# Kernel optimization log

Measured on AMD Instinct MI355X. Metric: run time of the kernel, lower is better.

The kernel has to match this reference:

```python
import jax, jax.numpy as jnp
import numpy as np

HIDDEN = 1024
HEADS = 16
HEAD_DIM = HIDDEN // HEADS
B, S = 2, 1024


def setup_inputs() -> dict:
    key = jax.random.key(0)
    ks = jax.random.split(key, 14)
    sc = 1.0 / np.sqrt(HIDDEN)
    inp = {
        "q": jax.random.normal(ks[0], (B, S, HIDDEN), jnp.float32),
        "k": jax.random.normal(ks[1], (B, S, HIDDEN), jnp.float32),
        "v": jax.random.normal(ks[2], (B, S, HIDDEN), jnp.float32),
        "mask": jax.random.randint(ks[3], (B, S), 0, 2, jnp.int32),
        "shift": jax.random.normal(ks[4], (B * HEADS, S, S), jnp.float32) * 0.1,
        "wq": jax.random.normal(ks[5], (HIDDEN, HIDDEN), jnp.float32) * sc,
        "bq": jnp.zeros((HIDDEN,), jnp.float32),
        "wk": jax.random.normal(ks[6], (HIDDEN, HIDDEN), jnp.float32) * sc,
        "bk": jnp.zeros((HIDDEN,), jnp.float32),
        "wv": jax.random.normal(ks[7], (HIDDEN, HIDDEN), jnp.float32) * sc,
        "bv": jnp.zeros((HIDDEN,), jnp.float32),
        "wo": jax.random.normal(ks[8], (HIDDEN, HIDDEN), jnp.float32) * sc,
        "bo": jnp.zeros((HIDDEN,), jnp.float32),
    }
    return inp


def _to_heads(x):
    # (B,S,Dm) -> (B*H, S, Dh), batch-major over heads (b*H + h)
    b, s, _ = x.shape
    return x.reshape(b, s, HEADS, HEAD_DIM).transpose(0, 2, 1, 3).reshape(b * HEADS, s, HEAD_DIM)


def reference(q, k, v, mask, shift, wq, bq, wk, bk, wv, bv, wo, bo):
    b, s, dm = q.shape
    qh = _to_heads(q @ wq.T + bq)
    kh = _to_heads(k @ wk.T + bk)
    vh = _to_heads(v @ wv.T + bv)
    scores = jnp.einsum("bqd,bkd->bqk", qh, kh) / jnp.float32(np.sqrt(HEAD_DIM))
    scores = scores + shift
    # faithful to torch: mask tiled head-major (h*B + b) -> outer product m_i * m_j
    m = jnp.tile(mask, (HEADS, 1))  # (H*B, S)
    attn_mask = m[:, :, None] * m[:, None, :]  # (H*B, S, S)
    scores = jnp.where(attn_mask == 0, jnp.float32(-1e9), scores)
    p = jax.nn.softmax(scores, axis=-1)
    out = jnp.einsum("bqk,bkd->bqd", p, vh)
    out = out.reshape(b, HEADS, s, HEAD_DIM).transpose(0, 2, 1, 3).reshape(b, s, dm)
    return out @ wo.T + bo
```

## Files before the change

kernel.cpp:

```cpp
#include <hip/hip_runtime.h>
#include <hip/hip_bf16.h>

#define S_LEN 1024
#define DMODEL 1024
#define N_HEADS 16
#define D_HEAD 64
#define BATCH 2
#define N_BH 32

typedef __attribute__((ext_vector_type(8))) short short8;
typedef __attribute__((ext_vector_type(4))) float f32x4;
typedef __attribute__((ext_vector_type(4))) int i32x4;

static __device__ __forceinline__ unsigned short f2bf(float x) {
    unsigned int u = __float_as_uint(x);
    return (unsigned short)((u + 0x7fffu + ((u >> 16) & 1u)) >> 16);
}

template <int AMODE>
__device__ __forceinline__ void gemm_body(const void* __restrict__ Araw,
                                          const float* __restrict__ W,
                                          const float* __restrict__ bias,
                                          void* __restrict__ outp, int outmode,
                                          int n0, int j0)
{
    __shared__ unsigned short As[128 * 40];
    __shared__ unsigned short Bs[64 * 40];
    const int t = threadIdx.x;
    const int lane = t & 63, w = t >> 6;
    const int wm = w >> 1, wn = w & 1;
    const int g = lane >> 4, r = lane & 15;

    f32x4 acc[4][2];
#pragma unroll
    for (int mi = 0; mi < 4; ++mi)
#pragma unroll
        for (int ni = 0; ni < 2; ++ni)
            acc[mi][ni] = (f32x4){0.f, 0.f, 0.f, 0.f};

    for (int ks = 0; ks < DMODEL / 32; ++ks) {
        const int k0 = ks * 32;
        __syncthreads();
        if (AMODE == 0) {
            const float* A = (const float*)Araw;
#pragma unroll
            for (int i = 0; i < 4; ++i) {
                int row = (t >> 3) + i * 32;
                int quad = t & 7;
                float4 f = *reinterpret_cast<const float4*>(A + (size_t)(n0 + row) * DMODEL + k0 + quad * 4);
                ushort4 hv = { f2bf(f.x), f2bf(f.y), f2bf(f.z), f2bf(f.w) };
                *reinterpret_cast<ushort4*>(&As[row * 40 + quad * 4]) = hv;
            }
        } else {
            const unsigned short* A = (const unsigned short*)Araw;
#pragma unroll
            for (int i = 0; i < 2; ++i) {
                int row = (t >> 2) + i * 64;
                int seg = t & 3;
                short8 v8 = *reinterpret_cast<const short8*>(A + (size_t)(n0 + row) * DMODEL + k0 + seg * 8);
                *reinterpret_cast<short8*>(&As[row * 40 + seg * 8]) = v8;
            }
        }
#pragma unroll
        for (int i = 0; i < 2; ++i) {
            int row = (t >> 3) + i * 32;
            int quad = t & 7;
            float4 f = *reinterpret_cast<const float4*>(W + (size_t)(j0 + row) * DMODEL + k0 + quad * 4);
            ushort4 hv = { f2bf(f.x), f2bf(f.y), f2bf(f.z), f2bf(f.w) };
            *reinterpret_cast<ushort4*>(&Bs[row * 40 + quad * 4]) = hv;
        }
        __syncthreads();
        short8 af[4], bfr[2];
#pragma unroll
        for (int mi = 0; mi < 4; ++mi)
            af[mi] = *reinterpret_cast<const short8*>(&As[(wm * 64 + mi * 16 + r) * 40 + g * 8]);
#pragma unroll
        for (int ni = 0; ni < 2; ++ni)
            bfr[ni] = *reinterpret_cast<const short8*>(&Bs[(wn * 32 + ni * 16 + r) * 40 + g * 8]);
#pragma unroll
        for (int mi = 0; mi < 4; ++mi)
#pragma unroll
            for (int ni = 0; ni < 2; ++ni)
                acc[mi][ni] = __builtin_amdgcn_mfma_f32_16x16x32_bf16(af[mi], bfr[ni], acc[mi][ni], 0, 0, 0);
    }

#pragma unroll
    for (int mi = 0; mi < 4; ++mi) {
#pragma unroll
        for (int ni = 0; ni < 2; ++ni) {
            int col = j0 + wn * 32 + ni * 16 + r;
            float bv = bias[col];
#pragma unroll
            for (int t4 = 0; t4 < 4; ++t4) {
                int n = n0 + wm * 64 + mi * 16 + g * 4 + t4;
                float v = acc[mi][ni][t4] + bv;
                if (outmode == 2) {
                    ((float*)outp)[(size_t)n * DMODEL + col] = v;
                } else {
                    int b_ = n >> 10, s_ = n & 1023;
                    int h_ = col >> 6, dh = col & 63;
                    if (outmode == 0)
                        ((unsigned short*)outp)[((size_t)(b_ * N_HEADS + h_) * S_LEN + s_) * D_HEAD + dh] = f2bf(v);
                    else
                        ((unsigned short*)outp)[((size_t)(b_ * N_HEADS + h_) * D_HEAD + dh) * S_LEN + s_] = f2bf(v);
                }
            }
        }
    }
}

__global__ __launch_bounds__(256) void qkv_kernel(
    const float* __restrict__ qx, const float* __restrict__ kx, const float* __restrict__ vx,
    const float* __restrict__ wq, const float* __restrict__ wk, const float* __restrict__ wv,
    const float* __restrict__ bq, const float* __restrict__ bk, const float* __restrict__ bv,
    unsigned short* Qh, unsigned short* Kh, unsigned short* Vt)
{
    const int z = blockIdx.z;
    const float* A    = (z == 0) ? qx : (z == 1) ? kx : vx;
    const float* W    = (z == 0) ? wq : (z == 1) ? wk : wv;
    const float* bias = (z == 0) ? bq : (z == 1) ? bk : bv;
    void* outp = (z == 0) ? (void*)Qh : (z == 1) ? (void*)Kh : (void*)Vt;
    gemm_body<0>(A, W, bias, outp, (z == 2) ? 1 : 0, blockIdx.x * 128, blockIdx.y * 64);
}

__global__ __launch_bounds__(256) void oproj_kernel(
    const unsigned short* __restrict__ attn, const float* __restrict__ wo,
    const float* __restrict__ bo, float* out)
{
    gemm_body<1>(attn, wo, bo, (void*)out, 2, blockIdx.x * 128, blockIdx.y * 64);
}

__global__ __launch_bounds__(256, 4) void attn_kernel(
    const unsigned short* __restrict__ Qh, const unsigned short* __restrict__ Kh,
    const unsigned short* __restrict__ Vt, const int* __restrict__ mask,
    const float* __restrict__ shift, unsigned short* __restrict__ attnbuf)
{
    __shared__ __align__(16) char smem[17408];
    __shared__ float Lw[4][16];
    auto Plds = reinterpret_cast<unsigned short(*)[16][72]>(smem);
    auto Olds = reinterpret_cast<float(*)[16][68]>(smem);

    const int f = blockIdx.x;
    const int l = (f & 7) * 256 + (f >> 3);
    const int bh = l >> 6, qg = l & 63;
    const int b_ = bh >> 4, h_ = bh & 15;
    const int t = threadIdx.x, w = t >> 6, lane = t & 63;
    const int g = lane >> 4, r = lane & 15;
    const int q0 = qg * 16;
    const int kstart = w * 256;

    const unsigned short* Qb = Qh + (size_t)bh * S_LEN * D_HEAD;
    const unsigned short* Kb = Kh + (size_t)bh * S_LEN * D_HEAD;
    const unsigned short* Vb = Vt + (size_t)bh * D_HEAD * S_LEN;
    const float* shb = shift + (size_t)bh * S_LEN * S_LEN;
    const int* mp = mask + (bh & (BATCH - 1)) * S_LEN;

    short8 qf0 = *reinterpret_cast<const short8*>(&Qb[(size_t)(q0 + r) * D_HEAD + g * 8]);
    short8 qf1 = *reinterpret_cast<const short8*>(&Qb[(size_t)(q0 + r) * D_HEAD + 32 + g * 8]);
    const int mq = mp[q0 + r];
    const float* shp = shb + (size_t)(q0 + r) * S_LEN + kstart;

    float l_loc = 0.f;
    f32x4 o_acc[4];
#pragma unroll
    for (int i = 0; i < 4; ++i) o_acc[i] = (f32x4){0.f, 0.f, 0.f, 0.f};

    f32x4 shA[4], shB[4];
#pragma unroll
    for (int fn = 0; fn < 4; ++fn) {
        shA[fn] = *reinterpret_cast<const f32x4*>(shp + fn * 16 + g * 4);
        shB[fn] = *reinterpret_cast<const f32x4*>(shp + 64 + fn * 16 + g * 4);
    }

#pragma unroll
    for (int kt = 0; kt < 4; ++kt) {
        const int kbase = kstart + kt * 64;
        const bool useA = (kt & 1) == 0;

#pragma unroll
        for (int fn = 0; fn < 4; ++fn) {
            short8 kv0 = *reinterpret_cast<const short8*>(&Kb[(size_t)(kbase + fn * 16 + r) * D_HEAD + g * 8]);
            short8 kv1 = *reinterpret_cast<const short8*>(&Kb[(size_t)(kbase + fn * 16 + r) * D_HEAD + 32 + g * 8]);
            f32x4 a = (f32x4){0.f, 0.f, 0.f, 0.f};
            a = __builtin_amdgcn_mfma_f32_16x16x32_bf16(kv0, qf0, a, 0, 0, 0);
            a = __builtin_amdgcn_mfma_f32_16x16x32_bf16(kv1, qf1, a, 0, 0, 0);
            f32x4 shv = useA ? shA[fn] : shB[fn];
            i32x4 mk = *reinterpret_cast<const i32x4*>(mp + kbase + fn * 16 + g * 4);
            float p0 = (mq & mk[0]) ? __expf(fmaf(a[0], 0.125f, shv[0])) : 0.f;
            float p1 = (mq & mk[1]) ? __expf(fmaf(a[1], 0.125f, shv[1])) : 0.f;
            float p2 = (mq & mk[2]) ? __expf(fmaf(a[2], 0.125f, shv[2])) : 0.f;
            float p3 = (mq & mk[3]) ? __expf(fmaf(a[3], 0.125f, shv[3])) : 0.f;
            if (mq == 0) { p0 = p1 = p2 = p3 = 1.f; }
            l_loc += (p0 + p1) + (p2 + p3);
            ushort4 pk = { f2bf(p0), f2bf(p1), f2bf(p2), f2bf(p3) };
            *reinterpret_cast<ushort4*>(&Plds[w][r][fn * 16 + g * 4]) = pk;
        }

        if (kt < 2) {
#pragma unroll
            for (int fn = 0; fn < 4; ++fn) {
                f32x4 nv = *reinterpret_cast<const f32x4*>(shp + (kt + 2) * 64 + fn * 16 + g * 4);
                if (useA) shA[fn] = nv; else shB[fn] = nv;
            }
        }

        short8 vfa[8];
#pragma unroll
        for (int df = 0; df < 4; ++df) {
            vfa[2 * df]     = *reinterpret_cast<const short8*>(&Vb[(size_t)(df * 16 + r) * S_LEN + kbase + g * 8]);
            vfa[2 * df + 1] = *reinterpret_cast<const short8*>(&Vb[(size_t)(df * 16 + r) * S_LEN + kbase + 32 + g * 8]);
        }

        asm volatile("s_waitcnt lgkmcnt(0)" ::: "memory");
        __builtin_amdgcn_sched_barrier(0);
        short8 pf0 = *reinterpret_cast<const short8*>(&Plds[w][r][g * 8]);
        short8 pf1 = *reinterpret_cast<const short8*>(&Plds[w][r][32 + g * 8]);
#pragma unroll
        for (int df = 0; df < 4; ++df) {
            o_acc[df] = __builtin_amdgcn_mfma_f32_16x16x32_bf16(pf0, vfa[2 * df], o_acc[df], 0, 0, 0);
            o_acc[df] = __builtin_amdgcn_mfma_f32_16x16x32_bf16(pf1, vfa[2 * df + 1], o_acc[df], 0, 0, 0);
        }
    }

    l_loc += __shfl_xor(l_loc, 16);
    l_loc += __shfl_xor(l_loc, 32);

    __syncthreads();

    if (g == 0) Lw[w][r] = l_loc;
#pragma unroll
    for (int df = 0; df < 4; ++df)
#pragma unroll
        for (int t4 = 0; t4 < 4; ++t4)
            Olds[w][g * 4 + t4][df * 16 + r] = o_acc[df][t4];

    __syncthreads();

    {
        const int col = t & 63;
        const int rb = t >> 6;
#pragma unroll
        for (int i = 0; i < 4; ++i) {
            int row = rb * 4 + i;
            float L = Lw[0][row] + Lw[1][row] + Lw[2][row] + Lw[3][row];
            float o = Olds[0][row][col] + Olds[1][row][col] + Olds[2][row][col] + Olds[3][row][col];
            attnbuf[(size_t)(b_ * S_LEN + q0 + row) * DMODEL + h_ * D_HEAD + col] = f2bf(o / L);
        }
    }
}

extern "C" void kernel_launch(void* const* d_in, const int* in_sizes, int n_in,
                              void* d_out, int out_size, void* d_ws, size_t ws_size,
                              hipStream_t stream)
{
    const float* q     = (const float*)d_in[0];
    const float* k     = (const float*)d_in[1];
    const float* v     = (const float*)d_in[2];
    const int*   mask  = (const int*)d_in[3];
    const float* shift = (const float*)d_in[4];
    const float* wq    = (const float*)d_in[5];
    const float* bq    = (const float*)d_in[6];
    const float* wk    = (const float*)d_in[7];
    const float* bk    = (const float*)d_in[8];
    const float* wv    = (const float*)d_in[9];
    const float* bv    = (const float*)d_in[10];
    const float* wo    = (const float*)d_in[11];
    const float* bo    = (const float*)d_in[12];
    float* out = (float*)d_out;

    const size_t nhalf = (size_t)N_BH * S_LEN * D_HEAD;
    unsigned short* Qh = (unsigned short*)d_ws;
    unsigned short* Kh = Qh + nhalf;
    unsigned short* Vt = Kh + nhalf;
    unsigned short* attnbuf = Vt + nhalf;

    dim3 blk(256);
    qkv_kernel<<<dim3(16, 16, 3), blk, 0, stream>>>(q, k, v, wq, wk, wv, bq, bk, bv, Qh, Kh, Vt);
    attn_kernel<<<dim3(2048), blk, 0, stream>>>(Qh, Kh, Vt, mask, shift, attnbuf);
    oproj_kernel<<<dim3(16, 16), blk, 0, stream>>>(attnbuf, wo, bo, out);
}
```

Before: 154.7 us.

## Stage shift tiles through double-buffered LDS with coalesced row loads

Shift values are now loaded cooperatively with full-row coalesced float4 reads into a swizzled, double-buffered LDS tile of 16x256 floats. Each wave now covers a strided 64-key chunk per iteration instead of a contiguous 256-key range. This is meant to replace the scattered per-lane 16-byte reads of the streaming shift tensor, which dominates memory traffic, with fully coalesced 1KB row segments. The cost is 32KB more LDS, extra block-wide barriers each iteration, and dropping the occupancy hint from launch bounds, so fewer blocks may fit per CU.

```diff
diff --git a/kernel.cpp b/kernel.cpp
--- a/kernel.cpp
+++ b/kernel.cpp
@@ -130,11 +130,12 @@
     gemm_body<1>(attn, wo, bo, (void*)out, 2, blockIdx.x * 128, blockIdx.y * 64);
 }
 
-__global__ __launch_bounds__(256, 4) void attn_kernel(
+__global__ __launch_bounds__(256) void attn_kernel(
     const unsigned short* __restrict__ Qh, const unsigned short* __restrict__ Kh,
     const unsigned short* __restrict__ Vt, const int* __restrict__ mask,
     const float* __restrict__ shift, unsigned short* __restrict__ attnbuf)
 {
+    __shared__ __align__(16) float Sh[2][16 * 256];
     __shared__ __align__(16) char smem[17408];
     __shared__ float Lw[4][16];
     auto Plds = reinterpret_cast<unsigned short(*)[16][72]>(smem);
@@ -147,7 +148,6 @@
     const int t = threadIdx.x, w = t >> 6, lane = t & 63;
     const int g = lane >> 4, r = lane & 15;
     const int q0 = qg * 16;
-    const int kstart = w * 256;
 
     const unsigned short* Qb = Qh + (size_t)bh * S_LEN * D_HEAD;
     const unsigned short* Kb = Kh + (size_t)bh * S_LEN * D_HEAD;
@@ -158,24 +158,38 @@
     short8 qf0 = *reinterpret_cast<const short8*>(&Qb[(size_t)(q0 + r) * D_HEAD + g * 8]);
     short8 qf1 = *reinterpret_cast<const short8*>(&Qb[(size_t)(q0 + r) * D_HEAD + 32 + g * 8]);
     const int mq = mp[q0 + r];
-    const float* shp = shb + (size_t)(q0 + r) * S_LEN + kstart;
 
     float l_loc = 0.f;
     f32x4 o_acc[4];
 #pragma unroll
     for (int i = 0; i < 4; ++i) o_acc[i] = (f32x4){0.f, 0.f, 0.f, 0.f};
 
-    f32x4 shA[4], shB[4];
-#pragma unroll
-    for (int fn = 0; fn < 4; ++fn) {
-        shA[fn] = *reinterpret_cast<const f32x4*>(shp + fn * 16 + g * 4);
-        shB[fn] = *reinterpret_cast<const f32x4*>(shp + 64 + fn * 16 + g * 4);
-    }
+    f32x4 stg[4];
+#pragma unroll
+    for (int i = 0; i < 4; ++i) {
+        int row = i * 4 + w;
+        stg[i] = *reinterpret_cast<const f32x4*>(shb + (size_t)(q0 + row) * S_LEN + lane * 4);
+    }
+#pragma unroll
+    for (int i = 0; i < 4; ++i) {
+        int row = i * 4 + w;
+        *reinterpret_cast<f32x4*>(&Sh[0][row * 256 + (lane ^ (row & 15)) * 4]) = stg[i];
+    }
+    __syncthreads();
 
 #pragma unroll
     for (int kt = 0; kt < 4; ++kt) {
-        const int kbase = kstart + kt * 64;
-        const bool useA = (kt & 1) == 0;
+        const int cur = kt & 1;
+        const int kbase = kt * 256 + w * 64;
+
+        if (kt < 3) {
+#pragma unroll
+            for (int i = 0; i < 4; ++i) {
+                int row = i * 4 + w;
+                stg[i] = *reinterpret_cast<const f32x4*>(
+                    shb + (size_t)(q0 + row) * S_LEN + (kt + 1) * 256 + lane * 4);
+            }
+        }
 
 #pragma unroll
         for (int fn = 0; fn < 4; ++fn) {
@@ -184,7 +198,8 @@
             f32x4 a = (f32x4){0.f, 0.f, 0.f, 0.f};
             a = __builtin_amdgcn_mfma_f32_16x16x32_bf16(kv0, qf0, a, 0, 0, 0);
             a = __builtin_amdgcn_mfma_f32_16x16x32_bf16(kv1, qf1, a, 0, 0, 0);
-            f32x4 shv = useA ? shA[fn] : shB[fn];
+            int slot = ((w << 4) | (fn << 2) | g) ^ (r & 15);
+            f32x4 shv = *reinterpret_cast<const f32x4*>(&Sh[cur][r * 256 + slot * 4]);
             i32x4 mk = *reinterpret_cast<const i32x4*>(mp + kbase + fn * 16 + g * 4);
             float p0 = (mq & mk[0]) ? __expf(fmaf(a[0], 0.125f, shv[0])) : 0.f;
             float p1 = (mq & mk[1]) ? __expf(fmaf(a[1], 0.125f, shv[1])) : 0.f;
@@ -196,14 +211,6 @@
             *reinterpret_cast<ushort4*>(&Plds[w][r][fn * 16 + g * 4]) = pk;
         }
 
-        if (kt < 2) {
-#pragma unroll
-            for (int fn = 0; fn < 4; ++fn) {
-                f32x4 nv = *reinterpret_cast<const f32x4*>(shp + (kt + 2) * 64 + fn * 16 + g * 4);
-                if (useA) shA[fn] = nv; else shB[fn] = nv;
-            }
-        }
-
         short8 vfa[8];
 #pragma unroll
         for (int df = 0; df < 4; ++df) {
@@ -219,6 +226,16 @@
         for (int df = 0; df < 4; ++df) {
             o_acc[df] = __builtin_amdgcn_mfma_f32_16x16x32_bf16(pf0, vfa[2 * df], o_acc[df], 0, 0, 0);
             o_acc[df] = __builtin_amdgcn_mfma_f32_16x16x32_bf16(pf1, vfa[2 * df + 1], o_acc[df], 0, 0, 0);
+        }
+
+        if (kt < 3) {
+            __syncthreads();
+#pragma unroll
+            for (int i = 0; i < 4; ++i) {
+                int row = i * 4 + w;
+                *reinterpret_cast<f32x4*>(&Sh[cur ^ 1][row * 256 + (lane ^ (row & 15)) * 4]) = stg[i];
+            }
+            __syncthreads();
         }
     }
 
```

New measurement: 141.8 us. -8.4%, faster.
